# Optimization experiments

Measured on AMD Instinct MI355X. Metric: run time of the kernel, lower is better.

Reference implementation:

```python
import jax, jax.numpy as jnp
import numpy as np

B, L, E, H = 2, 2048, 2048, 16
HD = E // H  # 128


def build_rope(length, head_dim, base=10000.0):
    # [L, head_dim//2, 2] with [..., 0]=sin, [..., 1]=cos (matches apply_rope indexing)
    half = head_dim // 2
    inv_freq = 1.0 / (base ** (jnp.arange(half, dtype=jnp.float32) * 2.0 / head_dim))
    ang = jnp.arange(length, dtype=jnp.float32)[:, None] * inv_freq[None, :]  # [L, half]
    return jnp.stack([jnp.sin(ang), jnp.cos(ang)], axis=-1)  # [L, half, 2]


def apply_rope(x, rope):
    # x: [B, L, H, D]; rope: [L, D//2, 2] (sin, cos)
    b, l, h, d = x.shape
    sin = rope[:, :, 0].reshape(1, l, 1, d // 2)
    cos = rope[:, :, 1].reshape(1, l, 1, d // 2)
    xr = x.reshape(b, l, h, d // 2, 2)
    q0, q1 = xr[..., 0], xr[..., 1]
    out = jnp.stack([q0 * cos - q1 * sin, q1 * cos + q0 * sin], axis=-1)
    return out.reshape(b, l, h, d)


def setup_inputs() -> dict:
    key = jax.random.key(0)
    k1, k2, k3 = jax.random.split(key, 3)
    x = jax.random.normal(k1, (B, L, E), dtype=jnp.float32)
    w_attn = jax.random.normal(k2, (3 * E, E), dtype=jnp.float32) * (E ** -0.5)
    w_proj = jax.random.normal(k3, (E, E), dtype=jnp.float32) * (E ** -0.5)
    rope = build_rope(L, HD)
    return {"x": x, "rope": rope, "w_attn": w_attn, "w_proj": w_proj}


def reference(x, rope, w_attn, w_proj):
    b, l, e = x.shape
    h, hd = H, HD
    qkv = jnp.einsum('ble,fe->blf', x, w_attn)  # [B, L, 3E]
    q, k, v = jnp.split(qkv, 3, axis=-1)
    q = apply_rope(q.reshape(b, l, h, hd), rope)
    k = apply_rope(k.reshape(b, l, h, hd), rope)
    v = v.reshape(b, l, h, hd)
    # causal SDPA, scale 1/sqrt(head_dim)
    scale = 1.0 / np.sqrt(hd).astype(np.float32)
    scores = jnp.einsum('bqhd,bkhd->bhqk', q, k) * scale
    causal = jnp.tril(jnp.ones((l, l), dtype=bool))
    scores = jnp.where(causal[None, None], scores, jnp.finfo(scores.dtype).min)
    att = jax.nn.softmax(scores, axis=-1)
    y = jnp.einsum('bhqk,bkhd->bqhd', att, v).reshape(b, l, e)
    return jnp.einsum('ble,fe->blf', y, w_proj)
```

## Files before the change

### kernel.cpp

```cpp
#include <hip/hip_runtime.h>
#include <math.h>

#define BATCH 2
#define LSEQ  2048
#define EMB   2048
#define NH    16
#define HD    128

typedef __attribute__((ext_vector_type(8))) short bf16x8;
typedef __attribute__((ext_vector_type(8))) unsigned short u16x8;
typedef __attribute__((ext_vector_type(4))) float f32x4;

static __device__ __forceinline__ unsigned short f2bf(float f) {
    unsigned u = __float_as_uint(f);
    u += 0x7fffu + ((u >> 16) & 1u);
    return (unsigned short)(u >> 16);
}

static __device__ __forceinline__ void load_lds16(const void* g, void* l) {
    __builtin_amdgcn_global_load_lds(
        (const __attribute__((address_space(1))) void*)g,
        (__attribute__((address_space(3))) void*)l, 16, 0, 0);
}

#define N1 (BATCH * LSEQ * EMB)
#define N2 (3 * EMB * EMB)
#define N3 (EMB * EMB)

__global__ __launch_bounds__(256) void cast_bf16_kernel(
    const float* __restrict__ x, const float* __restrict__ wa,
    const float* __restrict__ wp,
    unsigned short* __restrict__ xb, unsigned short* __restrict__ wab,
    unsigned short* __restrict__ wpb)
{
    size_t i4 = ((size_t)blockIdx.x * 256 + threadIdx.x) * 4;
    const float* src;
    unsigned short* dst;
    size_t off;
    if (i4 < (size_t)N1) { src = x; dst = xb; off = i4; }
    else if (i4 < (size_t)N1 + N2) { src = wa; dst = wab; off = i4 - N1; }
    else { src = wp; dst = wpb; off = i4 - N1 - N2; }
    float4 f = *(const float4*)(src + off);
    ushort4 u;
    u.x = f2bf(f.x); u.y = f2bf(f.y); u.z = f2bf(f.z); u.w = f2bf(f.w);
    *(ushort4*)(dst + off) = u;
}

template<int MI, int NI>
__global__ __launch_bounds__(512, 2) void gemm_bt_bf16(
    const unsigned short* __restrict__ A, const unsigned short* __restrict__ B,
    const float* __restrict__ rope,
    float* __restrict__ C,
    unsigned short* __restrict__ qo, unsigned short* __restrict__ ko,
    unsigned short* __restrict__ vo,
    int M, int N, int K, int mode)
{
    constexpr int BM = MI * 32;
    constexpr int BN = NI * 64;
    __shared__ __align__(16) unsigned short As[2][BM * 64];
    __shared__ __align__(16) unsigned short Bs[2][BN * 64];

    const int tid = threadIdx.x;
    const int lane = tid & 63;
    const int w = tid >> 6;
    const int m = lane & 15;
    const int g = lane >> 4;
    const int wr = w >> 2;
    const int wc = w & 3;
    const int sw = m & 7;

    const int nwgx = gridDim.x;
    const int lin = blockIdx.y * nwgx + blockIdx.x;
    const int cpx = (nwgx * gridDim.y) >> 3;
    const int swz = (lin & 7) * cpx + (lin >> 3);
    const int bm = (swz / nwgx) * BM;
    const int bn = (swz % nwgx) * BN;

    auto stage = [&](int buf, int k0) {
#pragma unroll
        for (int i = 0; i < MI / 2; i++) {
            const int idx = i * 512 + tid;
            const int row = idx >> 3;
            const int c = (idx & 7) ^ (row & 7);
            load_lds16(A + (size_t)(bm + row) * K + k0 + c * 8, &As[buf][idx * 8]);
        }
#pragma unroll
        for (int i = 0; i < NI; i++) {
            const int idx = i * 512 + tid;
            const int row = idx >> 3;
            const int c = (idx & 7) ^ (row & 7);
            load_lds16(B + (size_t)(bn + row) * K + k0 + c * 8, &Bs[buf][idx * 8]);
        }
    };

    f32x4 acc[MI][NI];
#pragma unroll
    for (int mi = 0; mi < MI; mi++)
#pragma unroll
        for (int ni = 0; ni < NI; ni++) acc[mi][ni] = (f32x4){0.f, 0.f, 0.f, 0.f};

    const int nt = K >> 6;
    constexpr int P = MI / 2;

    stage(0, 0);
    asm volatile("s_waitcnt vmcnt(0)" ::: "memory");
    __builtin_amdgcn_s_barrier();

    for (int t = 0; t < nt; t++) {
        const int rd = t & 1;
        const unsigned short* Ac = As[rd];
        const unsigned short* Bc = Bs[rd];
        bf16x8 bfv[NI][2];

#pragma unroll
        for (int p = 0; p < P; p++) {
            if (p == 0 && t + 1 < nt) stage(rd ^ 1, (t + 1) * 64);

            bf16x8 af[2][2];
#pragma unroll
            for (int mi2 = 0; mi2 < 2; mi2++) {
                const int row = wr * (MI * 16) + (p * 2 + mi2) * 16 + m;
#pragma unroll
                for (int kc = 0; kc < 2; kc++)
                    af[mi2][kc] = *(const bf16x8*)&Ac[(row * 8 + ((kc * 4 + g) ^ sw)) * 8];
            }
            if (p == 0) {
#pragma unroll
                for (int ni = 0; ni < NI; ni++) {
                    const int row = wc * (NI * 16) + ni * 16 + m;
#pragma unroll
                    for (int kc = 0; kc < 2; kc++)
                        bfv[ni][kc] = *(const bf16x8*)&Bc[(row * 8 + ((kc * 4 + g) ^ sw)) * 8];
                }
            }

            __builtin_amdgcn_s_barrier();
            asm volatile("s_waitcnt lgkmcnt(0)" ::: "memory");
            __builtin_amdgcn_s_setprio(1);
#pragma unroll
            for (int mi2 = 0; mi2 < 2; mi2++)
#pragma unroll
                for (int ni = 0; ni < NI; ni++)
#pragma unroll
                    for (int kc = 0; kc < 2; kc++)
                        acc[p * 2 + mi2][ni] = __builtin_amdgcn_mfma_f32_16x16x32_bf16(
                            af[mi2][kc], bfv[ni][kc], acc[p * 2 + mi2][ni], 0, 0, 0);
            __builtin_amdgcn_s_setprio(0);
            if (p == P - 1) {
                asm volatile("s_waitcnt vmcnt(0)" ::: "memory");
            }
            __builtin_amdgcn_s_barrier();
        }
    }

#pragma unroll
    for (int mi = 0; mi < MI; mi++) {
#pragma unroll
        for (int ni = 0; ni < NI; ni++) {
            const int col = bn + wc * (NI * 16) + ni * 16 + m;
            if (mode == 0) {
#pragma unroll
                for (int r = 0; r < 4; r++) {
                    const int row = bm + wr * (MI * 16) + mi * 16 + g * 4 + r;
                    C[(size_t)row * N + col] = acc[mi][ni][r];
                }
            } else {
                const int which = col >> 11;
                const int e = col & 2047;
                const int h = e >> 7;
                const int d = e & 127;
                if (which < 2) {
                    unsigned short* dst = (which == 0) ? qo : ko;
                    const int t2 = ((d >> 1) << 1);
#pragma unroll
                    for (int r = 0; r < 4; r++) {
                        const int row = bm + wr * (MI * 16) + mi * 16 + g * 4 + r;
                        const int b = row >> 11;
                        const int l = row & 2047;
                        float val = acc[mi][ni][r];
                        const float prt = __shfl_xor(val, 1);
                        const float2 sc = *(const float2*)(rope + (size_t)l * HD + t2);
                        val = (m & 1) ? fmaf(val, sc.y, prt * sc.x)
                                      : fmaf(val, sc.y, -prt * sc.x);
                        dst[(((size_t)(b * NH + h)) * LSEQ + l) * HD + d] = f2bf(val);
                    }
                } else {
                    const int l0 = bm + wr * (MI * 16) + mi * 16 + g * 4;
                    const int b = l0 >> 11;
                    const int l = l0 & 2047;
                    ushort4 vv;
                    vv.x = f2bf(acc[mi][ni][0]);
                    vv.y = f2bf(acc[mi][ni][1]);
                    vv.z = f2bf(acc[mi][ni][2]);
                    vv.w = f2bf(acc[mi][ni][3]);
                    *(ushort4*)(vo + (((size_t)(b * NH + h)) * HD + d) * LSEQ + l) = vv;
                }
            }
        }
    }
}

#define PTILES 32
#define PS_STR 68

__global__ __launch_bounds__(256) void attn_kernel(
    const unsigned short* __restrict__ q, const unsigned short* __restrict__ k,
    const unsigned short* __restrict__ vT, unsigned short* __restrict__ y)
{
    __shared__ __align__(16) unsigned short Ks[2][64 * 128];
    __shared__ __align__(16) unsigned short Vs[2][64 * 128];
    __shared__ __align__(16) unsigned short Ps[64 * PS_STR];

    const int tid = threadIdx.x;
    const int lane = tid & 63;
    const int w = tid >> 6;
    const int m = lane & 15;
    const int g = lane >> 4;
    const int bh = blockIdx.x;
    const int qt = PTILES - 1 - blockIdx.y;
    const int q0 = qt * 64;
    const size_t base = (size_t)bh * LSEQ * HD;
    const float scale = 0.08838834764831845f;
    const int bB = bh / NH;
    const int hh = bh % NH;
    const int sw = m & 7;

    auto stage = [&](int buf, int kb0) {
        const unsigned short* ksrc = k + base + (size_t)kb0 * HD;
#pragma unroll
        for (int i = 0; i < 4; i++) {
            const int idx = i * 256 + tid;
            const int row = idx >> 4;
            const int c = (idx & 15) ^ (row & 7);
            load_lds16(ksrc + (size_t)row * HD + c * 8, &Ks[buf][idx * 8]);
        }
#pragma unroll
        for (int i = 0; i < 4; i++) {
            const int idx = i * 256 + tid;
            const int d = idx >> 3;
            const int c = (idx & 7) ^ (d & 7);
            load_lds16(vT + base + (size_t)d * LSEQ + kb0 + c * 8, &Vs[buf][idx * 8]);
        }
    };

    bf16x8 aq[4];
    {
        const unsigned short* qrow = q + base + (size_t)(q0 + w * 16 + m) * HD;
#pragma unroll
        for (int kc = 0; kc < 4; kc++)
            aq[kc] = *(const bf16x8*)(qrow + kc * 32 + g * 8);
    }

    f32x4 o[8];
#pragma unroll
    for (int i = 0; i < 8; i++) o[i] = (f32x4){0.f, 0.f, 0.f, 0.f};
    float mprev[4], lsum[4];
#pragma unroll
    for (int r = 0; r < 4; r++) { mprev[r] = -1e30f; lsum[r] = 0.f; }

    stage(0, 0);
    int cur = 0;

    for (int kt = 0; kt <= qt; kt++) {
        const int k0 = kt * 64;

        __syncthreads();

        if (kt < qt) stage(cur ^ 1, k0 + 64);

        const unsigned short* Kc = Ks[cur];
        const unsigned short* Vc = Vs[cur];

        f32x4 s[4];
#pragma unroll
        for (int n = 0; n < 4; n++) {
            f32x4 acc = (f32x4){0.f, 0.f, 0.f, 0.f};
#pragma unroll
            for (int kc = 0; kc < 4; kc++) {
                const int row = n * 16 + m;
                bf16x8 bk = *(const bf16x8*)&Kc[(row * 16 + ((kc * 4 + g) ^ sw)) * 8];
                acc = __builtin_amdgcn_mfma_f32_16x16x32_bf16(aq[kc], bk, acc, 0, 0, 0);
            }
            s[n] = acc;
        }

        const int rowg = q0 + w * 16 + g * 4;
        if (kt == qt) {
#pragma unroll
            for (int n = 0; n < 4; n++) {
                const int col = k0 + n * 16 + m;
#pragma unroll
                for (int r = 0; r < 4; r++) {
                    const float val = s[n][r] * scale;
                    s[n][r] = (col <= rowg + r) ? val : -1e30f;
                }
            }
        } else {
#pragma unroll
            for (int n = 0; n < 4; n++)
#pragma unroll
                for (int r = 0; r < 4; r++) s[n][r] *= scale;
        }

        float al[4];
#pragma unroll
        for (int r = 0; r < 4; r++) {
            float v0 = fmaxf(fmaxf(s[0][r], s[1][r]), fmaxf(s[2][r], s[3][r]));
            v0 = fmaxf(v0, __shfl_xor(v0, 1));
            v0 = fmaxf(v0, __shfl_xor(v0, 2));
            v0 = fmaxf(v0, __shfl_xor(v0, 4));
            v0 = fmaxf(v0, __shfl_xor(v0, 8));
            const float mn = fmaxf(mprev[r], v0);
            al[r] = __expf(mprev[r] - mn);
            mprev[r] = mn;
        }
#pragma unroll
        for (int r = 0; r < 4; r++) {
            float sum = 0.f;
#pragma unroll
            for (int n = 0; n < 4; n++) {
                const float p = __expf(s[n][r] - mprev[r]);
                sum += p;
                Ps[(w * 16 + g * 4 + r) * PS_STR + n * 16 + m] = f2bf(p);
            }
            sum += __shfl_xor(sum, 1);
            sum += __shfl_xor(sum, 2);
            sum += __shfl_xor(sum, 4);
            sum += __shfl_xor(sum, 8);
            lsum[r] = lsum[r] * al[r] + sum;
        }

#pragma unroll
        for (int dc = 0; dc < 8; dc++)
#pragma unroll
            for (int r = 0; r < 4; r++) o[dc][r] *= al[r];

        bf16x8 ap[2];
#pragma unroll
        for (int kk = 0; kk < 2; kk++)
            ap[kk] = *(const bf16x8*)&Ps[(w * 16 + m) * PS_STR + kk * 32 + g * 8];
#pragma unroll
        for (int dc = 0; dc < 8; dc++) {
#pragma unroll
            for (int kk = 0; kk < 2; kk++) {
                const int row = dc * 16 + m;
                bf16x8 bv = *(const bf16x8*)&Vc[(row * 8 + ((kk * 4 + g) ^ sw)) * 8];
                o[dc] = __builtin_amdgcn_mfma_f32_16x16x32_bf16(ap[kk], bv, o[dc], 0, 0, 0);
            }
        }

        cur ^= 1;
    }

#pragma unroll
    for (int r = 0; r < 4; r++) {
        const float inv = 1.f / lsum[r];
        const int lrow = q0 + w * 16 + g * 4 + r;
        unsigned short* dst = y + (((size_t)bB * LSEQ + lrow) * NH + hh) * HD;
#pragma unroll
        for (int dc = 0; dc < 8; dc++)
            dst[dc * 16 + m] = f2bf(o[dc][r] * inv);
    }
}

extern "C" void kernel_launch(void* const* d_in, const int* in_sizes, int n_in,
                              void* d_out, int out_size, void* d_ws, size_t ws_size,
                              hipStream_t stream) {
    const float* x      = (const float*)d_in[0];
    const float* rope   = (const float*)d_in[1];
    const float* w_attn = (const float*)d_in[2];
    const float* w_proj = (const float*)d_in[3];
    float* out = (float*)d_out;
    unsigned short* ws = (unsigned short*)d_ws;

    const size_t per = (size_t)BATCH * NH * LSEQ * HD;
    unsigned short* qb  = ws;
    unsigned short* kb  = ws + per;
    unsigned short* vb  = ws + 2 * per;
    unsigned short* yb  = ws + 3 * per;
    unsigned short* xb  = ws + 4 * per;
    unsigned short* wab = xb + (size_t)N1;
    unsigned short* wpb = wab + (size_t)N2;

    const int M = BATCH * LSEQ;

    const int cast_blocks = (N1 + N2 + N3) / 4 / 256;
    cast_bf16_kernel<<<cast_blocks, 256, 0, stream>>>(x, w_attn, w_proj, xb, wab, wpb);

    dim3 g1(3 * EMB / 256, M / 128);
    gemm_bt_bf16<4, 4><<<g1, 512, 0, stream>>>(xb, wab, rope, nullptr, qb, kb, vb,
                                               M, 3 * EMB, EMB, 1);

    dim3 ga(BATCH * NH, PTILES);
    attn_kernel<<<ga, 256, 0, stream>>>(qb, kb, vb, yb);

    dim3 g2(EMB / 128, M / 256);
    gemm_bt_bf16<8, 2><<<g2, 512, 0, stream>>>(yb, wpb, nullptr, out,
                                               nullptr, nullptr, nullptr, M, EMB, EMB, 0);
}
```

Measured before the change: 450.6 us.

## Fix GEMM M-tile at 256 and software-pipeline LDS fragment reads with MFMA

The GEMM template now always uses a 256-row M tile with 8 accumulator rows per wave. The QKV projection moves from 128x256 to 256x256 tiles, halving its grid rows. The inner k-step loop is restructured to issue all global prefetches up front. A-fragment LDS reads are then double-buffered (afA/afB) and interleaved with MFMA phases using partial lgkmcnt waits and sched_barriers, which removes the per-phase block barriers. This aims to cut barrier stalls and hide LDS latency. The cost is more registers and LDS per block, which may lower occupancy, and fewer blocks for the QKV GEMM.

```diff
diff --git a/kernel.cpp b/kernel.cpp
--- a/kernel.cpp
+++ b/kernel.cpp
@@ -46,7 +46,7 @@
     *(ushort4*)(dst + off) = u;
 }
 
-template<int MI, int NI>
+template<int NI>
 __global__ __launch_bounds__(512, 2) void gemm_bt_bf16(
     const unsigned short* __restrict__ A, const unsigned short* __restrict__ B,
     const float* __restrict__ rope,
@@ -55,9 +55,8 @@
     unsigned short* __restrict__ vo,
     int M, int N, int K, int mode)
 {
-    constexpr int BM = MI * 32;
     constexpr int BN = NI * 64;
-    __shared__ __align__(16) unsigned short As[2][BM * 64];
+    __shared__ __align__(16) unsigned short As[2][256 * 64];
     __shared__ __align__(16) unsigned short Bs[2][BN * 64];
 
     const int tid = threadIdx.x;
@@ -73,12 +72,12 @@
     const int lin = blockIdx.y * nwgx + blockIdx.x;
     const int cpx = (nwgx * gridDim.y) >> 3;
     const int swz = (lin & 7) * cpx + (lin >> 3);
-    const int bm = (swz / nwgx) * BM;
+    const int bm = (swz / nwgx) * 256;
     const int bn = (swz % nwgx) * BN;
 
     auto stage = [&](int buf, int k0) {
 #pragma unroll
-        for (int i = 0; i < MI / 2; i++) {
+        for (int i = 0; i < 4; i++) {
             const int idx = i * 512 + tid;
             const int row = idx >> 3;
             const int c = (idx & 7) ^ (row & 7);
@@ -93,14 +92,13 @@
         }
     };
 
-    f32x4 acc[MI][NI];
-#pragma unroll
-    for (int mi = 0; mi < MI; mi++)
+    f32x4 acc[8][NI];
+#pragma unroll
+    for (int mi = 0; mi < 8; mi++)
 #pragma unroll
         for (int ni = 0; ni < NI; ni++) acc[mi][ni] = (f32x4){0.f, 0.f, 0.f, 0.f};
 
     const int nt = K >> 6;
-    constexpr int P = MI / 2;
 
     stage(0, 0);
     asm volatile("s_waitcnt vmcnt(0)" ::: "memory");
@@ -110,58 +108,78 @@
         const int rd = t & 1;
         const unsigned short* Ac = As[rd];
         const unsigned short* Bc = Bs[rd];
+
+        if (t + 1 < nt) stage(rd ^ 1, (t + 1) * 64);
+
+        bf16x8 afA[2][2], afB[2][2];
+#define READ_AF(dstv, pconst)                                                   \
+        {                                                                       \
+            _Pragma("unroll")                                                   \
+            for (int mi2 = 0; mi2 < 2; mi2++) {                                 \
+                const int row = wr * 128 + ((pconst) * 2 + mi2) * 16 + m;       \
+                _Pragma("unroll")                                               \
+                for (int kc = 0; kc < 2; kc++)                                  \
+                    dstv[mi2][kc] = *(const bf16x8*)&Ac[(row * 8 +              \
+                        ((kc * 4 + g) ^ sw)) * 8];                              \
+            }                                                                   \
+        }
+#define MFMA_PH(srcv, pconst)                                                   \
+        {                                                                       \
+            _Pragma("unroll")                                                   \
+            for (int mi2 = 0; mi2 < 2; mi2++)                                   \
+                _Pragma("unroll")                                               \
+                for (int ni = 0; ni < NI; ni++)                                 \
+                    _Pragma("unroll")                                           \
+                    for (int kc = 0; kc < 2; kc++)                              \
+                        acc[(pconst) * 2 + mi2][ni] =                           \
+                            __builtin_amdgcn_mfma_f32_16x16x32_bf16(            \
+                                srcv[mi2][kc], bfv[ni][kc],                     \
+                                acc[(pconst) * 2 + mi2][ni], 0, 0, 0);          \
+        }
+
         bf16x8 bfv[NI][2];
-
-#pragma unroll
-        for (int p = 0; p < P; p++) {
-            if (p == 0 && t + 1 < nt) stage(rd ^ 1, (t + 1) * 64);
-
-            bf16x8 af[2][2];
-#pragma unroll
-            for (int mi2 = 0; mi2 < 2; mi2++) {
-                const int row = wr * (MI * 16) + (p * 2 + mi2) * 16 + m;
-#pragma unroll
-                for (int kc = 0; kc < 2; kc++)
-                    af[mi2][kc] = *(const bf16x8*)&Ac[(row * 8 + ((kc * 4 + g) ^ sw)) * 8];
-            }
-            if (p == 0) {
-#pragma unroll
-                for (int ni = 0; ni < NI; ni++) {
-                    const int row = wc * (NI * 16) + ni * 16 + m;
-#pragma unroll
-                    for (int kc = 0; kc < 2; kc++)
-                        bfv[ni][kc] = *(const bf16x8*)&Bc[(row * 8 + ((kc * 4 + g) ^ sw)) * 8];
-                }
-            }
-
-            __builtin_amdgcn_s_barrier();
-            asm volatile("s_waitcnt lgkmcnt(0)" ::: "memory");
-            __builtin_amdgcn_s_setprio(1);
-#pragma unroll
-            for (int mi2 = 0; mi2 < 2; mi2++)
-#pragma unroll
-                for (int ni = 0; ni < NI; ni++)
-#pragma unroll
-                    for (int kc = 0; kc < 2; kc++)
-                        acc[p * 2 + mi2][ni] = __builtin_amdgcn_mfma_f32_16x16x32_bf16(
-                            af[mi2][kc], bfv[ni][kc], acc[p * 2 + mi2][ni], 0, 0, 0);
-            __builtin_amdgcn_s_setprio(0);
-            if (p == P - 1) {
-                asm volatile("s_waitcnt vmcnt(0)" ::: "memory");
-            }
-            __builtin_amdgcn_s_barrier();
-        }
+#pragma unroll
+        for (int ni = 0; ni < NI; ni++) {
+            const int row = wc * (NI * 16) + ni * 16 + m;
+#pragma unroll
+            for (int kc = 0; kc < 2; kc++)
+                bfv[ni][kc] = *(const bf16x8*)&Bc[(row * 8 + ((kc * 4 + g) ^ sw)) * 8];
+        }
+        READ_AF(afA, 0)
+        asm volatile("s_waitcnt lgkmcnt(0)" ::: "memory");
+        __builtin_amdgcn_sched_barrier(0);
+
+        __builtin_amdgcn_s_setprio(1);
+        READ_AF(afB, 1)
+        MFMA_PH(afA, 0)
+        READ_AF(afA, 2)
+        asm volatile("s_waitcnt lgkmcnt(4)" ::: "memory");
+        __builtin_amdgcn_sched_barrier(0);
+        MFMA_PH(afB, 1)
+        READ_AF(afB, 3)
+        asm volatile("s_waitcnt lgkmcnt(4)" ::: "memory");
+        __builtin_amdgcn_sched_barrier(0);
+        MFMA_PH(afA, 2)
+        asm volatile("s_waitcnt lgkmcnt(0)" ::: "memory");
+        __builtin_amdgcn_sched_barrier(0);
+        MFMA_PH(afB, 3)
+        __builtin_amdgcn_s_setprio(0);
+
+        asm volatile("s_waitcnt vmcnt(0)" ::: "memory");
+        __builtin_amdgcn_s_barrier();
+#undef READ_AF
+#undef MFMA_PH
     }
 
 #pragma unroll
-    for (int mi = 0; mi < MI; mi++) {
+    for (int mi = 0; mi < 8; mi++) {
 #pragma unroll
         for (int ni = 0; ni < NI; ni++) {
             const int col = bn + wc * (NI * 16) + ni * 16 + m;
             if (mode == 0) {
 #pragma unroll
                 for (int r = 0; r < 4; r++) {
-                    const int row = bm + wr * (MI * 16) + mi * 16 + g * 4 + r;
+                    const int row = bm + wr * 128 + mi * 16 + g * 4 + r;
                     C[(size_t)row * N + col] = acc[mi][ni][r];
                 }
             } else {
@@ -174,7 +192,7 @@
                     const int t2 = ((d >> 1) << 1);
 #pragma unroll
                     for (int r = 0; r < 4; r++) {
-                        const int row = bm + wr * (MI * 16) + mi * 16 + g * 4 + r;
+                        const int row = bm + wr * 128 + mi * 16 + g * 4 + r;
                         const int b = row >> 11;
                         const int l = row & 2047;
                         float val = acc[mi][ni][r];
@@ -185,7 +203,7 @@
                         dst[(((size_t)(b * NH + h)) * LSEQ + l) * HD + d] = f2bf(val);
                     }
                 } else {
-                    const int l0 = bm + wr * (MI * 16) + mi * 16 + g * 4;
+                    const int l0 = bm + wr * 128 + mi * 16 + g * 4;
                     const int b = l0 >> 11;
                     const int l = l0 & 2047;
                     ushort4 vv;
@@ -387,14 +405,14 @@
     const int cast_blocks = (N1 + N2 + N3) / 4 / 256;
     cast_bf16_kernel<<<cast_blocks, 256, 0, stream>>>(x, w_attn, w_proj, xb, wab, wpb);
 
-    dim3 g1(3 * EMB / 256, M / 128);
-    gemm_bt_bf16<4, 4><<<g1, 512, 0, stream>>>(xb, wab, rope, nullptr, qb, kb, vb,
-                                               M, 3 * EMB, EMB, 1);
+    dim3 g1(3 * EMB / 256, M / 256);
+    gemm_bt_bf16<4><<<g1, 512, 0, stream>>>(xb, wab, rope, nullptr, qb, kb, vb,
+                                            M, 3 * EMB, EMB, 1);
 
     dim3 ga(BATCH * NH, PTILES);
     attn_kernel<<<ga, 256, 0, stream>>>(qb, kb, vb, yb);
 
     dim3 g2(EMB / 128, M / 256);
-    gemm_bt_bf16<8, 2><<<g2, 512, 0, stream>>>(yb, wpb, nullptr, out,
-                                               nullptr, nullptr, nullptr, M, EMB, EMB, 0);
-}
+    gemm_bt_bf16<2><<<g2, 512, 0, stream>>>(yb, wpb, nullptr, out,
+                                            nullptr, nullptr, nullptr, M, EMB, EMB, 0);
+}
```

Result: faster. 417.1 us (-7.4%).
